# Optimization experiments

Measured on AMD Instinct MI355X. Metric: run time of the kernel, lower is better.

Reference implementation:

```python
import jax, jax.numpy as jnp
import numpy as np

E = 1024
H = 8
D = E // H
B = 16384
LN_EPS = 1e-5


def setup_inputs() -> dict:
    key = jax.random.key(0)
    ks = jax.random.split(key, 12)
    s = 1.0 / np.sqrt(E)
    return {
        "image_features": jax.random.normal(ks[0], (B, E), jnp.float32),
        "signal_features": jax.random.normal(ks[1], (B, E), jnp.float32),
        "Wq": jax.random.normal(ks[2], (E, E), jnp.float32) * s,
        "Wk": jax.random.normal(ks[3], (E, E), jnp.float32) * s,
        "Wv": jax.random.normal(ks[4], (E, E), jnp.float32) * s,
        "bq": jnp.zeros((E,), jnp.float32),
        "bk": jnp.zeros((E,), jnp.float32),
        "bv": jnp.zeros((E,), jnp.float32),
        "Wo": jax.random.normal(ks[5], (E, E), jnp.float32) * s,
        "bo": jnp.zeros((E,), jnp.float32),
        "ln_gamma": jnp.ones((E,), jnp.float32),
        "ln_beta": jnp.zeros((E,), jnp.float32),
    }


def _forward(image_features, signal_features, Wq, Wk, Wv, bq, bk, bv, Wo, bo, ln_gamma, ln_beta):
    # query: [B,1,E] from image; key/value: [B,2,E] stacked modalities
    kv = jnp.stack([image_features, signal_features], axis=1)  # [B,2,E]
    # projections (torch Linear convention: x @ W^T + b)
    q = (image_features @ Wq.T + bq).reshape(B, H, 1, D)       # [B,H,1,D]
    k = (kv @ Wk.T + bk).reshape(B, 2, H, D).transpose(0, 2, 1, 3)  # [B,H,2,D]
    v = (kv @ Wv.T + bv).reshape(B, 2, H, D).transpose(0, 2, 1, 3)  # [B,H,2,D]
    scale = 1.0 / jnp.sqrt(jnp.float32(D))
    scores = jnp.einsum("bhqd,bhkd->bhqk", q, k) * scale       # [B,H,1,2]
    attn = jax.nn.softmax(scores, axis=-1)
    ctx = jnp.einsum("bhqk,bhkd->bhqd", attn, v)               # [B,H,1,D]
    ctx = ctx.reshape(B, E)
    attn_out = ctx @ Wo.T + bo
    # residual + LayerNorm (dropout is identity in eval)
    fused = attn_out + image_features
    mu = jnp.mean(fused, axis=-1, keepdims=True)
    var = jnp.var(fused, axis=-1, keepdims=True)
    normed = (fused - mu) * jax.lax.rsqrt(var + LN_EPS)
    return normed * ln_gamma + ln_beta


def reference(image_features, signal_features, Wq, Wk, Wv, bq, bk, bv, Wo, bo, ln_gamma, ln_beta):
    return _forward(image_features, signal_features, Wq, Wk, Wv, bq, bk, bv, Wo, bo, ln_gamma, ln_beta)
```

## Files before the change

kernel.cpp:

```cpp
#include <hip/hip_runtime.h>

#define B_ 16384
#define E_ 1024
#define H_ 8
#define D_ 128

typedef _Float16 f16;
typedef _Float16 f16x8 __attribute__((ext_vector_type(8)));
typedef float f32x4 __attribute__((ext_vector_type(4)));

__device__ __forceinline__ void gload16(const f16* g, f16* l) {
    __builtin_amdgcn_global_load_lds(
        (const __attribute__((address_space(1))) void*)g,
        (__attribute__((address_space(3))) void*)l, 16, 0, 0);
}


__global__ __launch_bounds__(256) void cvt2_kernel(const float4* __restrict__ s0,
                                                   const float4* __restrict__ s1,
                                                   ushort4* __restrict__ d0,
                                                   ushort4* __restrict__ d1, int n4) {
    const float4* s = blockIdx.y ? s1 : s0;
    ushort4* d = blockIdx.y ? d1 : d0;
    int i = blockIdx.x * 256 + threadIdx.x;
    if (i >= n4) return;
    float4 v = s[i];
    union { ushort4 u; f16 h[4]; } o;
    o.h[0] = (f16)v.x; o.h[1] = (f16)v.y; o.h[2] = (f16)v.z; o.h[3] = (f16)v.w;
    d[i] = o.u;
}

__global__ __launch_bounds__(256) void cvt4_kernel(
    const float4* __restrict__ s0, const float4* __restrict__ s1,
    const float4* __restrict__ s2, const float4* __restrict__ s3,
    ushort4* __restrict__ d0, ushort4* __restrict__ d1,
    ushort4* __restrict__ d2, ushort4* __restrict__ d3, int n4) {
    const float4* s; ushort4* d;
    switch (blockIdx.y) {
        case 0: s = s0; d = d0; break;
        case 1: s = s1; d = d1; break;
        case 2: s = s2; d = d2; break;
        default: s = s3; d = d3; break;
    }
    int i = blockIdx.x * 256 + threadIdx.x;
    if (i >= n4) return;
    float4 v = s[i];
    union { ushort4 u; f16 h[4]; } o;
    o.h[0] = (f16)v.x; o.h[1] = (f16)v.y; o.h[2] = (f16)v.z; o.h[3] = (f16)v.w;
    d[i] = o.u;
}

__global__ __launch_bounds__(256, 2) void qkv_attn_kernel(
    const f16* __restrict__ Xi, const f16* __restrict__ Xs,
    const f16* __restrict__ Wq, const f16* __restrict__ Wk, const f16* __restrict__ Wv,
    const float* __restrict__ bq, const float* __restrict__ bk, const float* __restrict__ bv,
    f16* __restrict__ ctx)
{
    __shared__ f16 sAi[2][64][32];
    __shared__ f16 sAs[2][64][32];
    __shared__ f16 sWq[2][128][32];
    __shared__ f16 sWk[2][128][32];
    __shared__ f16 sWv[2][128][32];
    __shared__ float sdot[2][64][2];
    __shared__ float sa0[64];

    const int tid  = threadIdx.x;
    const int lane = tid & 63;
    const int wave = tid >> 6;
    const int wr = wave >> 1, wc = wave & 1;
    const int l16 = lane & 15, lq = lane >> 4;

    const int bid  = blockIdx.x;
    const int head = bid & 7;
    const int row0 = (bid >> 3) * 64;
    const int col0 = head * D_;

    const int lr = lane >> 2;
    const int lc = ((lane & 3) ^ ((lane >> 3) & 3)) * 8;
    const int rc = (lq ^ ((l16 >> 1) & 3)) * 8;

    const f16* gAi = Xi + (size_t)(row0 + wave * 16 + lr) * E_ + lc;
    const f16* gAs = Xs + (size_t)(row0 + wave * 16 + lr) * E_ + lc;
    const size_t woff = (size_t)(col0 + wave * 32 + lr) * E_ + lc;
    const f16* gWq = Wq + woff;
    const f16* gWk = Wk + woff;
    const f16* gWv = Wv + woff;
    const size_t wskip = (size_t)16 * E_;

    f32x4 zero4 = {0.f, 0.f, 0.f, 0.f};
    f32x4 accQ[2][4], accKi[2][4], accKs[2][4], accVi[2][4], accVs[2][4];
    #pragma unroll
    for (int i = 0; i < 2; i++)
        #pragma unroll
        for (int j = 0; j < 4; j++) {
            accQ[i][j] = zero4; accKi[i][j] = zero4; accKs[i][j] = zero4;
            accVi[i][j] = zero4; accVs[i][j] = zero4;
        }

    for (int kk = 0; kk < E_; kk += 64) {
        #pragma unroll
        for (int h = 0; h < 2; h++) {
            const int ko = kk + h * 32;
            gload16(gAi + ko,         &sAi[h][wave * 16][0]);
            gload16(gAs + ko,         &sAs[h][wave * 16][0]);
            gload16(gWq + ko,         &sWq[h][wave * 32][0]);
            gload16(gWq + wskip + ko, &sWq[h][wave * 32 + 16][0]);
            gload16(gWk + ko,         &sWk[h][wave * 32][0]);
            gload16(gWk + wskip + ko, &sWk[h][wave * 32 + 16][0]);
            gload16(gWv + ko,         &sWv[h][wave * 32][0]);
            gload16(gWv + wskip + ko, &sWv[h][wave * 32 + 16][0]);
        }
        __syncthreads();

        #pragma unroll
        for (int h = 0; h < 2; h++) {
            f16x8 aI[2], aS[2], bF[4];
            #pragma unroll
            for (int fr = 0; fr < 2; fr++) {
                aI[fr] = *(const f16x8*)&sAi[h][wr * 32 + fr * 16 + l16][rc];
                aS[fr] = *(const f16x8*)&sAs[h][wr * 32 + fr * 16 + l16][rc];
            }
            #pragma unroll
            for (int fc = 0; fc < 4; fc++)
                bF[fc] = *(const f16x8*)&sWq[h][wc * 64 + fc * 16 + l16][rc];
            #pragma unroll
            for (int fr = 0; fr < 2; fr++)
                #pragma unroll
                for (int fc = 0; fc < 4; fc++)
                    accQ[fr][fc] = __builtin_amdgcn_mfma_f32_16x16x32_f16(aI[fr], bF[fc], accQ[fr][fc], 0, 0, 0);
            #pragma unroll
            for (int fc = 0; fc < 4; fc++)
                bF[fc] = *(const f16x8*)&sWk[h][wc * 64 + fc * 16 + l16][rc];
            #pragma unroll
            for (int fr = 0; fr < 2; fr++)
                #pragma unroll
                for (int fc = 0; fc < 4; fc++) {
                    accKi[fr][fc] = __builtin_amdgcn_mfma_f32_16x16x32_f16(aI[fr], bF[fc], accKi[fr][fc], 0, 0, 0);
                    accKs[fr][fc] = __builtin_amdgcn_mfma_f32_16x16x32_f16(aS[fr], bF[fc], accKs[fr][fc], 0, 0, 0);
                }
            #pragma unroll
            for (int fc = 0; fc < 4; fc++)
                bF[fc] = *(const f16x8*)&sWv[h][wc * 64 + fc * 16 + l16][rc];
            #pragma unroll
            for (int fr = 0; fr < 2; fr++)
                #pragma unroll
                for (int fc = 0; fc < 4; fc++) {
                    accVi[fr][fc] = __builtin_amdgcn_mfma_f32_16x16x32_f16(aI[fr], bF[fc], accVi[fr][fc], 0, 0, 0);
                    accVs[fr][fc] = __builtin_amdgcn_mfma_f32_16x16x32_f16(aS[fr], bF[fc], accVs[fr][fc], 0, 0, 0);
                }
        }
        __syncthreads();
    }

    #pragma unroll
    for (int fc = 0; fc < 4; fc++) {
        int col = col0 + wc * 64 + fc * 16 + l16;
        float bqv = bq[col], bkv = bk[col];
        #pragma unroll
        for (int fr = 0; fr < 2; fr++)
            #pragma unroll
            for (int e = 0; e < 4; e++) {
                accQ[fr][fc][e]  += bqv;
                accKi[fr][fc][e] += bkv;
                accKs[fr][fc][e] += bkv;
            }
    }

    #pragma unroll
    for (int fr = 0; fr < 2; fr++)
        #pragma unroll
        for (int e = 0; e < 4; e++) {
            float d0 = 0.f, d1 = 0.f;
            #pragma unroll
            for (int fc = 0; fc < 4; fc++) {
                d0 += accQ[fr][fc][e] * accKi[fr][fc][e];
                d1 += accQ[fr][fc][e] * accKs[fr][fc][e];
            }
            #pragma unroll
            for (int m = 1; m < 16; m <<= 1) {
                d0 += __shfl_xor(d0, m, 64);
                d1 += __shfl_xor(d1, m, 64);
            }
            if (l16 == 0) {
                int row = wr * 32 + fr * 16 + lq * 4 + e;
                sdot[0][row][wc] = d0;
                sdot[1][row][wc] = d1;
            }
        }
    __syncthreads();
    if (tid < 64) {
        const float scale = 0.088388347648318447f;
        float s0 = (sdot[0][tid][0] + sdot[0][tid][1]) * scale;
        float s1 = (sdot[1][tid][0] + sdot[1][tid][1]) * scale;
        sa0[tid] = 1.0f / (1.0f + expf(s1 - s0));
    }
    __syncthreads();

    #pragma unroll
    for (int fc = 0; fc < 4; fc++) {
        int col = col0 + wc * 64 + fc * 16 + l16;
        float bvv = bv[col];
        #pragma unroll
        for (int fr = 0; fr < 2; fr++)
            #pragma unroll
            for (int e = 0; e < 4; e++) {
                int row = wr * 32 + fr * 16 + lq * 4 + e;
                float a0 = sa0[row];
                float v  = a0 * accVi[fr][fc][e] + (1.0f - a0) * accVs[fr][fc][e] + bvv;
                ctx[(size_t)(row0 + row) * E_ + col] = (f16)v;
            }
    }
}

__global__ __launch_bounds__(256, 4) void out_proj_kernel(
    const f16* __restrict__ A, const f16* __restrict__ Wo, const float* __restrict__ bo,
    f16* __restrict__ a16)
{
    __shared__ f16 sA[2][128][32];
    __shared__ f16 sB[2][128][32];
    const int tid  = threadIdx.x;
    const int lane = tid & 63;
    const int wave = tid >> 6;
    const int wr = wave >> 1, wc = wave & 1;
    const int l16 = lane & 15, lq = lane >> 4;

    const int bid  = blockIdx.x;
    const int col0 = (bid & 7) * 128;
    const int row0 = (bid >> 3) * 128;

    const int lr = lane >> 2;
    const int lc = ((lane & 3) ^ ((lane >> 3) & 3)) * 8;
    const int rc = (lq ^ ((l16 >> 1) & 3)) * 8;

    const f16* gA0 = A  + (size_t)(row0 + wave * 32 + lr) * E_ + lc;
    const f16* gB0 = Wo + (size_t)(col0 + wave * 32 + lr) * E_ + lc;
    const size_t wskip = (size_t)16 * E_;

    f32x4 zero4 = {0.f, 0.f, 0.f, 0.f};
    f32x4 acc[4][4];
    #pragma unroll
    for (int i = 0; i < 4; i++)
        #pragma unroll
        for (int j = 0; j < 4; j++) acc[i][j] = zero4;

    for (int kk = 0; kk < E_; kk += 64) {
        #pragma unroll
        for (int h = 0; h < 2; h++) {
            const int ko = kk + h * 32;
            gload16(gA0 + ko,         &sA[h][wave * 32][0]);
            gload16(gA0 + wskip + ko, &sA[h][wave * 32 + 16][0]);
            gload16(gB0 + ko,         &sB[h][wave * 32][0]);
            gload16(gB0 + wskip + ko, &sB[h][wave * 32 + 16][0]);
        }
        __syncthreads();

        #pragma unroll
        for (int h = 0; h < 2; h++) {
            f16x8 aF[4], bF[4];
            #pragma unroll
            for (int f = 0; f < 4; f++) {
                aF[f] = *(const f16x8*)&sA[h][wr * 64 + f * 16 + l16][rc];
                bF[f] = *(const f16x8*)&sB[h][wc * 64 + f * 16 + l16][rc];
            }
            #pragma unroll
            for (int fr = 0; fr < 4; fr++)
                #pragma unroll
                for (int fc = 0; fc < 4; fc++)
                    acc[fr][fc] = __builtin_amdgcn_mfma_f32_16x16x32_f16(aF[fr], bF[fc], acc[fr][fc], 0, 0, 0);
        }
        __syncthreads();
    }

    #pragma unroll
    for (int fc = 0; fc < 4; fc++) {
        int col = col0 + wc * 64 + fc * 16 + l16;
        float bov = bo[col];
        #pragma unroll
        for (int fr = 0; fr < 4; fr++)
            #pragma unroll
            for (int e = 0; e < 4; e++) {
                int row = row0 + wr * 64 + fr * 16 + lq * 4 + e;
                a16[(size_t)row * E_ + col] = (f16)(acc[fr][fc][e] + bov);
            }
    }
}

__global__ __launch_bounds__(256) void ln_kernel(
    const f16* __restrict__ a16, const f16* __restrict__ resid16,
    const float* __restrict__ gamma, const float* __restrict__ beta,
    float* __restrict__ out)
{
    const int row = blockIdx.x;
    const int tid = threadIdx.x;
    union { ushort4 u; f16 h[4]; } ua, ur;
    ua.u = ((const ushort4*)(a16     + (size_t)row * E_))[tid];
    ur.u = ((const ushort4*)(resid16 + (size_t)row * E_))[tid];
    float4 v;
    v.x = (float)ua.h[0] + (float)ur.h[0];
    v.y = (float)ua.h[1] + (float)ur.h[1];
    v.z = (float)ua.h[2] + (float)ur.h[2];
    v.w = (float)ua.h[3] + (float)ur.h[3];
    float s  = v.x + v.y + v.z + v.w;
    float s2 = v.x * v.x + v.y * v.y + v.z * v.z + v.w * v.w;
    #pragma unroll
    for (int m = 1; m < 64; m <<= 1) {
        s  += __shfl_xor(s, m, 64);
        s2 += __shfl_xor(s2, m, 64);
    }
    __shared__ float red[8];
    int wv = tid >> 6, ln = tid & 63;
    if (ln == 0) { red[wv] = s; red[4 + wv] = s2; }
    __syncthreads();
    s  = red[0] + red[1] + red[2] + red[3];
    s2 = red[4] + red[5] + red[6] + red[7];
    float mu  = s * (1.0f / E_);
    float var = s2 * (1.0f / E_) - mu * mu;
    float r   = rsqrtf(var + 1e-5f);
    float4 g  = ((const float4*)gamma)[tid];
    float4 bb = ((const float4*)beta)[tid];
    float4 o;
    o.x = (v.x - mu) * r * g.x + bb.x;
    o.y = (v.y - mu) * r * g.y + bb.y;
    o.z = (v.z - mu) * r * g.z + bb.z;
    o.w = (v.w - mu) * r * g.w + bb.w;
    ((float4*)(out + (size_t)row * E_))[tid] = o;
}

extern "C" void kernel_launch(void* const* d_in, const int* in_sizes, int n_in,
                              void* d_out, int out_size, void* d_ws, size_t ws_size,
                              hipStream_t stream)
{
    (void)in_sizes; (void)n_in; (void)out_size; (void)ws_size;
    const float* image  = (const float*)d_in[0];
    const float* signal = (const float*)d_in[1];
    const float* Wq = (const float*)d_in[2];
    const float* Wk = (const float*)d_in[3];
    const float* Wv = (const float*)d_in[4];
    const float* bq = (const float*)d_in[5];
    const float* bk = (const float*)d_in[6];
    const float* bv = (const float*)d_in[7];
    const float* Wo = (const float*)d_in[8];
    const float* bo = (const float*)d_in[9];
    const float* gamma = (const float*)d_in[10];
    const float* beta  = (const float*)d_in[11];
    float* out = (float*)d_out;

    char* ws = (char*)d_ws;
    f16* Xi16 = (f16*)(ws);
    f16* Xs16 = (f16*)(ws + 32ull * 1024 * 1024);
    f16* Wq16 = (f16*)(ws + 64ull * 1024 * 1024);
    f16* Wk16 = (f16*)(ws + 66ull * 1024 * 1024);
    f16* Wv16 = (f16*)(ws + 68ull * 1024 * 1024);
    f16* Wo16 = (f16*)(ws + 70ull * 1024 * 1024);
    f16* ctx  = (f16*)(ws + 72ull * 1024 * 1024);
    f16* a16  = Xs16;

    const int nBE4 = B_ * E_ / 4;
    const int nEE4 = E_ * E_ / 4;
    dim3 gX(nBE4 / 256, 2);
    cvt2_kernel<<<gX, 256, 0, stream>>>((const float4*)image, (const float4*)signal,
                                        (ushort4*)Xi16, (ushort4*)Xs16, nBE4);
    dim3 gW(nEE4 / 256, 4);
    cvt4_kernel<<<gW, 256, 0, stream>>>((const float4*)Wq, (const float4*)Wk,
                                        (const float4*)Wv, (const float4*)Wo,
                                        (ushort4*)Wq16, (ushort4*)Wk16,
                                        (ushort4*)Wv16, (ushort4*)Wo16, nEE4);

    qkv_attn_kernel<<<B_ / 64 * H_, 256, 0, stream>>>(Xi16, Xs16, Wq16, Wk16, Wv16,
                                                      bq, bk, bv, ctx);

    out_proj_kernel<<<B_ / 128 * 8, 256, 0, stream>>>(ctx, Wo16, bo, a16);

    ln_kernel<<<B_, 256, 0, stream>>>(a16, Xi16, gamma, beta, out);
}
```

Baseline: 438.7 us.

## Merge conversion kernels, reorder QKV grid, triple-buffer out-projection K loop

Merges the two fp32-to-fp16 conversion kernels into one launch that covers activations and all four weights. Changes the QKV/attention grid to 2D with row blocks on x and heads on y, so consecutive blocks share a head's weights instead of an activation tile. Rewrites the out-projection K loop as a 3-stage LDS pipeline with 32-wide K steps, using vmcnt waits and one barrier per step instead of two syncthreads per 64-wide step. The extra LDS buffer lowers the occupancy hint from 4 to 3 blocks per CU.

```diff
diff --git a/kernel.cpp b/kernel.cpp
--- a/kernel.cpp
+++ b/kernel.cpp
@@ -16,34 +16,30 @@
 }
 
 
-__global__ __launch_bounds__(256) void cvt2_kernel(const float4* __restrict__ s0,
-                                                   const float4* __restrict__ s1,
-                                                   ushort4* __restrict__ d0,
-                                                   ushort4* __restrict__ d1, int n4) {
-    const float4* s = blockIdx.y ? s1 : s0;
-    ushort4* d = blockIdx.y ? d1 : d0;
-    int i = blockIdx.x * 256 + threadIdx.x;
-    if (i >= n4) return;
-    float4 v = s[i];
-    union { ushort4 u; f16 h[4]; } o;
-    o.h[0] = (f16)v.x; o.h[1] = (f16)v.y; o.h[2] = (f16)v.z; o.h[3] = (f16)v.w;
-    d[i] = o.u;
-}
-
-__global__ __launch_bounds__(256) void cvt4_kernel(
-    const float4* __restrict__ s0, const float4* __restrict__ s1,
-    const float4* __restrict__ s2, const float4* __restrict__ s3,
-    ushort4* __restrict__ d0, ushort4* __restrict__ d1,
-    ushort4* __restrict__ d2, ushort4* __restrict__ d3, int n4) {
+__global__ __launch_bounds__(256) void cvt6_kernel(
+    const float4* __restrict__ xi, const float4* __restrict__ xs,
+    const float4* __restrict__ wq, const float4* __restrict__ wk,
+    const float4* __restrict__ wv, const float4* __restrict__ wo,
+    ushort4* __restrict__ dxi, ushort4* __restrict__ dxs,
+    ushort4* __restrict__ dwq, ushort4* __restrict__ dwk,
+    ushort4* __restrict__ dwv, ushort4* __restrict__ dwo)
+{
+    int b = blockIdx.x;
     const float4* s; ushort4* d;
-    switch (blockIdx.y) {
-        case 0: s = s0; d = d0; break;
-        case 1: s = s1; d = d1; break;
-        case 2: s = s2; d = d2; break;
-        default: s = s3; d = d3; break;
-    }
-    int i = blockIdx.x * 256 + threadIdx.x;
-    if (i >= n4) return;
+    if (b < 32768) {
+        if (b < 16384) { s = xi; d = dxi; }
+        else           { s = xs; d = dxs; b -= 16384; }
+    } else {
+        b -= 32768;
+        int w = b >> 10; b &= 1023;
+        switch (w) {
+            case 0:  s = wq; d = dwq; break;
+            case 1:  s = wk; d = dwk; break;
+            case 2:  s = wv; d = dwv; break;
+            default: s = wo; d = dwo; break;
+        }
+    }
+    size_t i = (size_t)b * 256 + threadIdx.x;
     float4 v = s[i];
     union { ushort4 u; f16 h[4]; } o;
     o.h[0] = (f16)v.x; o.h[1] = (f16)v.y; o.h[2] = (f16)v.z; o.h[3] = (f16)v.w;
@@ -70,10 +66,8 @@
     const int wr = wave >> 1, wc = wave & 1;
     const int l16 = lane & 15, lq = lane >> 4;
 
-    const int bid  = blockIdx.x;
-    const int head = bid & 7;
-    const int row0 = (bid >> 3) * 64;
-    const int col0 = head * D_;
+    const int row0 = blockIdx.x * 64;
+    const int col0 = blockIdx.y * D_;
 
     const int lr = lane >> 2;
     const int lc = ((lane & 3) ^ ((lane >> 3) & 3)) * 8;
@@ -212,12 +206,12 @@
     }
 }
 
-__global__ __launch_bounds__(256, 4) void out_proj_kernel(
+__global__ __launch_bounds__(256, 3) void out_proj_kernel(
     const f16* __restrict__ A, const f16* __restrict__ Wo, const float* __restrict__ bo,
     f16* __restrict__ a16)
 {
-    __shared__ f16 sA[2][128][32];
-    __shared__ f16 sB[2][128][32];
+    __shared__ f16 sA[3][128][32];
+    __shared__ f16 sB[3][128][32];
     const int tid  = threadIdx.x;
     const int lane = tid & 63;
     const int wave = tid >> 6;
@@ -243,32 +237,43 @@
         #pragma unroll
         for (int j = 0; j < 4; j++) acc[i][j] = zero4;
 
-    for (int kk = 0; kk < E_; kk += 64) {
-        #pragma unroll
-        for (int h = 0; h < 2; h++) {
-            const int ko = kk + h * 32;
-            gload16(gA0 + ko,         &sA[h][wave * 32][0]);
-            gload16(gA0 + wskip + ko, &sA[h][wave * 32 + 16][0]);
-            gload16(gB0 + ko,         &sB[h][wave * 32][0]);
-            gload16(gB0 + wskip + ko, &sB[h][wave * 32 + 16][0]);
-        }
-        __syncthreads();
-
-        #pragma unroll
-        for (int h = 0; h < 2; h++) {
-            f16x8 aF[4], bF[4];
-            #pragma unroll
-            for (int f = 0; f < 4; f++) {
-                aF[f] = *(const f16x8*)&sA[h][wr * 64 + f * 16 + l16][rc];
-                bF[f] = *(const f16x8*)&sB[h][wc * 64 + f * 16 + l16][rc];
-            }
-            #pragma unroll
-            for (int fr = 0; fr < 4; fr++)
-                #pragma unroll
-                for (int fc = 0; fc < 4; fc++)
-                    acc[fr][fc] = __builtin_amdgcn_mfma_f32_16x16x32_f16(aF[fr], bF[fc], acc[fr][fc], 0, 0, 0);
-        }
-        __syncthreads();
+    auto stage = [&](int b, int kk) {
+        gload16(gA0 + kk,         &sA[b][wave * 32][0]);
+        gload16(gA0 + wskip + kk, &sA[b][wave * 32 + 16][0]);
+        gload16(gB0 + kk,         &sB[b][wave * 32][0]);
+        gload16(gB0 + wskip + kk, &sB[b][wave * 32 + 16][0]);
+    };
+
+    stage(0, 0);
+    stage(1, 32);
+    asm volatile("s_waitcnt vmcnt(4)" ::: "memory");
+    __builtin_amdgcn_s_barrier();
+
+    const int NT = E_ / 32;
+    #pragma unroll
+    for (int t = 0; t < NT; ++t) {
+        const int cur = t % 3;
+        if (t + 2 < NT) stage((t + 2) % 3, (t + 2) * 32);
+
+        f16x8 aF[4], bF[4];
+        #pragma unroll
+        for (int f = 0; f < 4; f++) {
+            aF[f] = *(const f16x8*)&sA[cur][wr * 64 + f * 16 + l16][rc];
+            bF[f] = *(const f16x8*)&sB[cur][wc * 64 + f * 16 + l16][rc];
+        }
+        #pragma unroll
+        for (int fr = 0; fr < 4; fr++)
+            #pragma unroll
+            for (int fc = 0; fc < 4; fc++)
+                acc[fr][fc] = __builtin_amdgcn_mfma_f32_16x16x32_f16(aF[fr], bF[fc], acc[fr][fc], 0, 0, 0);
+
+        if (t + 2 < NT) {
+            asm volatile("s_waitcnt vmcnt(4)" ::: "memory");
+            __builtin_amdgcn_s_barrier();
+        } else if (t + 1 < NT) {
+            asm volatile("s_waitcnt vmcnt(0)" ::: "memory");
+            __builtin_amdgcn_s_barrier();
+        }
     }
 
     #pragma unroll
@@ -355,19 +360,15 @@
     f16* ctx  = (f16*)(ws + 72ull * 1024 * 1024);
     f16* a16  = Xs16;
 
-    const int nBE4 = B_ * E_ / 4;
-    const int nEE4 = E_ * E_ / 4;
-    dim3 gX(nBE4 / 256, 2);
-    cvt2_kernel<<<gX, 256, 0, stream>>>((const float4*)image, (const float4*)signal,
-                                        (ushort4*)Xi16, (ushort4*)Xs16, nBE4);
-    dim3 gW(nEE4 / 256, 4);
-    cvt4_kernel<<<gW, 256, 0, stream>>>((const float4*)Wq, (const float4*)Wk,
-                                        (const float4*)Wv, (const float4*)Wo,
-                                        (ushort4*)Wq16, (ushort4*)Wk16,
-                                        (ushort4*)Wv16, (ushort4*)Wo16, nEE4);
-
-    qkv_attn_kernel<<<B_ / 64 * H_, 256, 0, stream>>>(Xi16, Xs16, Wq16, Wk16, Wv16,
-                                                      bq, bk, bv, ctx);
+    cvt6_kernel<<<32768 + 4096, 256, 0, stream>>>(
+        (const float4*)image, (const float4*)signal,
+        (const float4*)Wq, (const float4*)Wk, (const float4*)Wv, (const float4*)Wo,
+        (ushort4*)Xi16, (ushort4*)Xs16,
+        (ushort4*)Wq16, (ushort4*)Wk16, (ushort4*)Wv16, (ushort4*)Wo16);
+
+    dim3 g2(B_ / 64, H_);
+    qkv_attn_kernel<<<g2, 256, 0, stream>>>(Xi16, Xs16, Wq16, Wk16, Wv16,
+                                            bq, bk, bv, ctx);
 
     out_proj_kernel<<<B_ / 128 * 8, 256, 0, stream>>>(ctx, Wo16, bo, a16);
 
```

New measurement: 454.6 us. +3.6%, slower.
